# Kernel optimization log

Measured on AMD Instinct MI355X. Metric: run time of the kernel, lower is better.

The kernel has to match this reference:

```python
import jax, jax.numpy as jnp
import numpy as np

N_NODES = 100000
NNZ = 3200000
D_FEAT = 128


def setup_inputs() -> dict:
    key = jax.random.key(0)
    k1, k2, k3 = jax.random.split(key, 3)
    indices = jax.random.randint(k1, (2, NNZ), 0, N_NODES, dtype=jnp.int64 if jax.config.jax_enable_x64 else jnp.int32)
    values = jax.random.normal(k2, (NNZ,), dtype=jnp.float32)
    b = jax.random.normal(k3, (N_NODES, D_FEAT), dtype=jnp.float32)
    return {"indices": indices, "values": values, "n_rows": N_NODES, "b": b}


def reference(indices, values, n_rows, b):
    # out = sparse_coo(indices, values, [n_rows, n_rows]) @ b
    # out[i] = sum_{e: row[e]==i} values[e] * b[col[e]]
    row, col = indices[0], indices[1]
    gathered = values[:, None] * b[col]              # [nnz, d]
    out = jax.ops.segment_sum(gathered, row, num_segments=n_rows)  # [n_rows, d]
    return out
```

## Files before the change

### kernel.cpp

```cpp
#include <hip/hip_runtime.h>


#define D_FEAT 128
#define RPB 128
#define BKT_SHIFT 7
#define MAX_NB 1024
#define NBLK_SCAT 512
#define CHUNK_MAX 6400
#define STG_CAP 6144
#define CT_SHIFT 13
#define NKEY (RPB * 16)
#define RP_FLAG (1 << 30)

__device__ __forceinline__ unsigned short f2bf(float f) {
    unsigned u = __float_as_uint(f);
    u += 0x7FFFu + ((u >> 16) & 1u);
    return (unsigned short)(u >> 16);
}
__global__ void bconv_kernel(const float* __restrict__ bmat,
                             ushort* __restrict__ b16, int n4) {
    int i = blockIdx.x * blockDim.x + threadIdx.x;
    int gs = gridDim.x * blockDim.x;
    for (int k = i; k < n4; k += gs) {
        float4 v = reinterpret_cast<const float4*>(bmat)[k];
        ushort4 o;
        o.x = f2bf(v.x); o.y = f2bf(v.y); o.z = f2bf(v.z); o.w = f2bf(v.w);
        reinterpret_cast<ushort4*>(b16)[k] = o;
    }
}

__global__ void hist_kernel(const int* __restrict__ rowidx, int* __restrict__ hist,
                            int nnz) {
    __shared__ int lcnt[MAX_NB];
    for (int i = threadIdx.x; i < MAX_NB; i += blockDim.x) lcnt[i] = 0;
    __syncthreads();
    int gid = blockIdx.x * blockDim.x + threadIdx.x;
    int gsz = gridDim.x * blockDim.x;
    for (int e = gid; e < nnz; e += gsz)
        atomicAdd(&lcnt[rowidx[e] >> BKT_SHIFT], 1);
    __syncthreads();
    for (int i = threadIdx.x; i < MAX_NB; i += blockDim.x)
        if (lcnt[i]) atomicAdd(&hist[i], lcnt[i]);
}

__global__ void scan_kernel(const int* __restrict__ hist, int* __restrict__ gbase,
                            int* __restrict__ gcursor, int nb) {
    __shared__ int hs[512];
    int t = threadIdx.x;
    int v0 = hist[2 * t], v1 = hist[2 * t + 1];
    hs[t] = v0 + v1;
    __syncthreads();
    for (int off = 1; off < 512; off <<= 1) {
        int u = (t >= off) ? hs[t - off] : 0;
        __syncthreads();
        hs[t] += u;
        __syncthreads();
    }
    int excl = hs[t] - (v0 + v1);
    if (2 * t < nb)     { gbase[2 * t] = excl;          gcursor[2 * t] = excl; }
    if (2 * t + 1 < nb) { gbase[2 * t + 1] = excl + v0; gcursor[2 * t + 1] = excl + v0; }
}

__global__ __launch_bounds__(512)
void scatter_kernel(const int* __restrict__ rowidx, const int* __restrict__ colidx,
                    const float* __restrict__ vals, int* __restrict__ gcursor,
                    float2* __restrict__ cv, int nnz, int nb) {
    __shared__ int loff[MAX_NB];
    __shared__ int cur[MAX_NB];
    __shared__ int gpos[MAX_NB];
    __shared__ ushort bktof[CHUNK_MAX];
    __shared__ float2 stage[CHUNK_MAX];
    int* scanbuf = (int*)stage;

    int t = threadIdx.x;
    int chunk = (nnz + gridDim.x - 1) / gridDim.x;
    int beg = blockIdx.x * chunk;
    int end = min(beg + chunk, nnz);
    int n = end - beg;

    for (int i = t; i < MAX_NB; i += 512) loff[i] = 0;
    __syncthreads();
    for (int e = beg + t; e < end; e += 512)
        atomicAdd(&loff[rowidx[e] >> BKT_SHIFT], 1);
    __syncthreads();

    int v0 = loff[2 * t], v1 = loff[2 * t + 1];
    scanbuf[t] = v0 + v1;
    __syncthreads();
    for (int off = 1; off < 512; off <<= 1) {
        int u = (t >= off) ? scanbuf[t - off] : 0;
        __syncthreads();
        scanbuf[t] += u;
        __syncthreads();
    }
    int excl = scanbuf[t] - (v0 + v1);
    __syncthreads();
    loff[2 * t] = excl;       loff[2 * t + 1] = excl + v0;
    cur[2 * t]  = excl;       cur[2 * t + 1]  = excl + v0;
    __syncthreads();

    for (int e = beg + t; e < end; e += 512) {
        int r = rowidx[e];
        int bkt = r >> BKT_SHIFT;
        int pos = atomicAdd(&cur[bkt], 1);
        int pack = ((r & (RPB - 1)) << 17) | colidx[e];
        stage[pos] = make_float2(__int_as_float(pack), vals[e]);
        bktof[pos] = (ushort)bkt;
    }
    __syncthreads();

    for (int i = t; i < nb; i += 512) {
        int cnt = cur[i] - loff[i];
        if (cnt > 0) gpos[i] = atomicAdd(&gcursor[i], cnt);
    }
    __syncthreads();

    for (int i = t; i < n; i += 512) {
        int bkt = bktof[i];
        cv[gpos[bkt] + (i - loff[bkt])] = stage[i];
    }
}

__global__ __launch_bounds__(256)
void rowsort_kernel(const int* __restrict__ gbase, const int* __restrict__ gend,
                    float2* __restrict__ cv, int* __restrict__ rowptr,
                    int n_rows, int nb) {
    __shared__ float2 stg[STG_CAP];
    __shared__ int bin[NKEY];
    __shared__ int cur[NKEY];
    __shared__ int part[256];
    int t = threadIdx.x;
    int bkt = blockIdx.x;
    int beg = gbase[bkt], end = gend[bkt];
    int n = end - beg;

    if (bkt == nb - 1 && t == 0) rowptr[n_rows] = end;

    if (n > STG_CAP) {
        for (int rl = t; rl < RPB; rl += 256) {
            int row = bkt * RPB + rl;
            if (row < n_rows) rowptr[row] = beg | RP_FLAG;
        }
        return;
    }

    for (int i = t; i < NKEY; i += 256) bin[i] = 0;
    __syncthreads();
    for (int i = t; i < n; i += 256) {
        float2 p = cv[beg + i];
        stg[i] = p;
        int pk = __float_as_int(p.x);
        int key = ((pk >> 17) << 4) | ((pk & 0x1FFFF) >> CT_SHIFT);
        atomicAdd(&bin[key], 1);
    }
    __syncthreads();
    int base8 = t * 8;
    int loc[8];
    int s = 0;
    #pragma unroll
    for (int k = 0; k < 8; ++k) { loc[k] = bin[base8 + k]; s += loc[k]; }
    part[t] = s;
    __syncthreads();
    for (int off = 1; off < 256; off <<= 1) {
        int u = (t >= off) ? part[t - off] : 0;
        __syncthreads();
        part[t] += u;
        __syncthreads();
    }
    int run = part[t] - s;
    #pragma unroll
    for (int k = 0; k < 8; ++k) {
        int key = base8 + k;
        cur[key] = run;
        if ((key & 15) == 0) {
            int row = bkt * RPB + (key >> 4);
            if (row < n_rows) rowptr[row] = beg + run;
        }
        run += loc[k];
    }
    __syncthreads();
    for (int i = t; i < n; i += 256) {
        float2 p = stg[i];
        int pk = __float_as_int(p.x);
        int key = ((pk >> 17) << 4) | ((pk & 0x1FFFF) >> CT_SHIFT);
        int pos = atomicAdd(&cur[key], 1);
        cv[beg + pos] = p;
    }
}

__device__ __forceinline__ float bf2f(unsigned short h) {
    return __uint_as_float((unsigned)h << 16);
}
__global__ __launch_bounds__(256)
void rowmm16_kernel(const int* __restrict__ rowptr, const int* __restrict__ gbase,
                    const int* __restrict__ gend, const float2* __restrict__ cv,
                    const ushort* __restrict__ b16, float* __restrict__ out,
                    int n_rows) {
    int wid  = (blockIdx.x * blockDim.x + threadIdx.x) >> 6;
    int lane = threadIdx.x & 63;
    if (wid >= n_rows) return;

    const ushort2* bp = reinterpret_cast<const ushort2*>(b16) + lane;
    float2 acc = make_float2(0.f, 0.f);

    int rp = rowptr[wid];
    if (rp & RP_FLAG) {
        int bkt = wid >> BKT_SHIFT;
        int beg = gbase[bkt], end = gend[bkt];
        int myrl = wid & (RPB - 1);
        for (int j = beg; j < end; ++j) {
            float2 p = cv[j];
            int pack = __float_as_int(p.x);
            if ((pack >> 17) == myrl) {
                ushort2 u = bp[(size_t)(pack & 0x1FFFF) * (D_FEAT / 2)];
                acc.x += p.y * bf2f(u.x);  acc.y += p.y * bf2f(u.y);
            }
        }
    } else {
        int beg = rp;
        int end = rowptr[wid + 1] & ~RP_FLAG;
        int j = beg;
        for (; j + 7 < end; j += 8) {
            float2 p0 = cv[j],     p1 = cv[j + 1];
            float2 p2 = cv[j + 2], p3 = cv[j + 3];
            float2 p4 = cv[j + 4], p5 = cv[j + 5];
            float2 p6 = cv[j + 6], p7 = cv[j + 7];
            ushort2 u0 = bp[(size_t)(__float_as_int(p0.x) & 0x1FFFF) * (D_FEAT / 2)];
            ushort2 u1 = bp[(size_t)(__float_as_int(p1.x) & 0x1FFFF) * (D_FEAT / 2)];
            ushort2 u2 = bp[(size_t)(__float_as_int(p2.x) & 0x1FFFF) * (D_FEAT / 2)];
            ushort2 u3 = bp[(size_t)(__float_as_int(p3.x) & 0x1FFFF) * (D_FEAT / 2)];
            ushort2 u4 = bp[(size_t)(__float_as_int(p4.x) & 0x1FFFF) * (D_FEAT / 2)];
            ushort2 u5 = bp[(size_t)(__float_as_int(p5.x) & 0x1FFFF) * (D_FEAT / 2)];
            ushort2 u6 = bp[(size_t)(__float_as_int(p6.x) & 0x1FFFF) * (D_FEAT / 2)];
            ushort2 u7 = bp[(size_t)(__float_as_int(p7.x) & 0x1FFFF) * (D_FEAT / 2)];
            acc.x += p0.y * bf2f(u0.x);  acc.y += p0.y * bf2f(u0.y);
            acc.x += p1.y * bf2f(u1.x);  acc.y += p1.y * bf2f(u1.y);
            acc.x += p2.y * bf2f(u2.x);  acc.y += p2.y * bf2f(u2.y);
            acc.x += p3.y * bf2f(u3.x);  acc.y += p3.y * bf2f(u3.y);
            acc.x += p4.y * bf2f(u4.x);  acc.y += p4.y * bf2f(u4.y);
            acc.x += p5.y * bf2f(u5.x);  acc.y += p5.y * bf2f(u5.y);
            acc.x += p6.y * bf2f(u6.x);  acc.y += p6.y * bf2f(u6.y);
            acc.x += p7.y * bf2f(u7.x);  acc.y += p7.y * bf2f(u7.y);
        }
        for (; j < end; ++j) {
            float2 p = cv[j];
            ushort2 u = bp[(size_t)(__float_as_int(p.x) & 0x1FFFF) * (D_FEAT / 2)];
            acc.x += p.y * bf2f(u.x);  acc.y += p.y * bf2f(u.y);
        }
    }
    reinterpret_cast<float2*>(out + (size_t)wid * D_FEAT)[lane] = acc;
}

__global__ __launch_bounds__(256)
void rowmm_kernel(const int* __restrict__ rowptr, const int* __restrict__ gbase,
                  const int* __restrict__ gend, const float2* __restrict__ cv,
                  const float* __restrict__ bmat, float* __restrict__ out,
                  int n_rows) {
    int wid  = (blockIdx.x * blockDim.x + threadIdx.x) >> 6;
    int lane = threadIdx.x & 63;
    if (wid >= n_rows) return;
    const float2* bp = reinterpret_cast<const float2*>(bmat) + lane;
    float2 acc = make_float2(0.f, 0.f);
    int rp = rowptr[wid];
    if (rp & RP_FLAG) {
        int bkt = wid >> BKT_SHIFT;
        int beg = gbase[bkt], end = gend[bkt];
        int myrl = wid & (RPB - 1);
        for (int j = beg; j < end; ++j) {
            float2 p = cv[j];
            int pack = __float_as_int(p.x);
            if ((pack >> 17) == myrl) {
                float2 v = bp[(size_t)(pack & 0x1FFFF) * (D_FEAT / 2)];
                acc.x += p.y * v.x;  acc.y += p.y * v.y;
            }
        }
    } else {
        int beg = rp, end = rowptr[wid + 1] & ~RP_FLAG;
        for (int j = beg; j < end; ++j) {
            float2 p = cv[j];
            float2 v = bp[(size_t)(__float_as_int(p.x) & 0x1FFFF) * (D_FEAT / 2)];
            acc.x += p.y * v.x;  acc.y += p.y * v.y;
        }
    }
    reinterpret_cast<float2*>(out + (size_t)wid * D_FEAT)[lane] = acc;
}

extern "C" void kernel_launch(void* const* d_in, const int* in_sizes, int n_in,
                              void* d_out, int out_size, void* d_ws, size_t ws_size,
                              hipStream_t stream) {
    const int*   indices = (const int*)d_in[0];
    const float* values  = (const float*)d_in[1];
    const float* b       = (const float*)d_in[3];
    float*       out     = (float*)d_out;

    const int nnz    = in_sizes[1];
    const int n_rows = out_size / D_FEAT;
    const int nb     = (n_rows + RPB - 1) / RPB;
    const int* rowidx = indices;
    const int* colidx = indices + nnz;

    int*    hist    = (int*)d_ws;
    int*    gbase   = hist + MAX_NB;
    int*    gcursor = gbase + MAX_NB;
    int*    rowptr  = gcursor + MAX_NB;
    size_t  off     = (3 * MAX_NB + (size_t)n_rows + 1) * sizeof(int);
    off = (off + 15) & ~(size_t)15;

    size_t b16_bytes = (size_t)n_rows * D_FEAT * sizeof(ushort);
    size_t cv_bytes  = (size_t)nnz * sizeof(float2);
    bool   use16     = (off + b16_bytes + cv_bytes) <= ws_size;

    ushort* b16 = (ushort*)((char*)d_ws + off);
    float2* cv  = (float2*)((char*)d_ws + off + (use16 ? b16_bytes : 0));

    hipMemsetAsync(hist, 0, MAX_NB * sizeof(int), stream);
    if (use16)
        bconv_kernel<<<1024, 256, 0, stream>>>(b, b16, n_rows * D_FEAT / 4);
    hist_kernel<<<512, 256, 0, stream>>>(rowidx, hist, nnz);
    scan_kernel<<<1, 512, 0, stream>>>(hist, gbase, gcursor, nb);
    scatter_kernel<<<NBLK_SCAT, 512, 0, stream>>>(rowidx, colidx, values, gcursor, cv, nnz, nb);
    rowsort_kernel<<<nb, 256, 0, stream>>>(gbase, gcursor, cv, rowptr, n_rows, nb);
    if (use16)
        rowmm16_kernel<<<(n_rows * 64 + 255) / 256, 256, 0, stream>>>(rowptr, gbase, gcursor,
                                                                      cv, b16, out, n_rows);
    else
        rowmm_kernel<<<(n_rows * 64 + 255) / 256, 256, 0, stream>>>(rowptr, gbase, gcursor,
                                                                    cv, b, out, n_rows);
}
```

Before: 251.9 us.

## Tile SpMM by column segment within 64-row buckets and add atomic fallback

Buckets shrink to 64 rows. Rowsort now orders each bucket's entries column-tile-major (16 column tiles by 64 rows) and stores per-bucket ushort offsets instead of a global rowptr. The new mm kernel assigns one block per bucket, and each warp owns 8 rows. All warps sweep the column tiles in the same order, so gathers of b rows stay in a smaller cache footprint. The change also adds an atomic fallback for oversized inputs and sizes the scatter grid by chunk size. The costs are more serial per-warp work, lower parallelism (about 1563 blocks), and loop overhead per row-tile segment.

```diff
diff --git a/kernel.cpp b/kernel.cpp
--- a/kernel.cpp
+++ b/kernel.cpp
@@ -2,21 +2,45 @@
 
 
 #define D_FEAT 128
-#define RPB 128
-#define BKT_SHIFT 7
-#define MAX_NB 1024
-#define NBLK_SCAT 512
+#define RPB 64
+#define BKT_SHIFT 6
+#define MAX_NB 2048
 #define CHUNK_MAX 6400
-#define STG_CAP 6144
+#define STG_CAP 3072
+#define NT 16
 #define CT_SHIFT 13
-#define NKEY (RPB * 16)
-#define RP_FLAG (1 << 30)
+#define NKEY 1024
+#define SSTRIDE 1025
 
 __device__ __forceinline__ unsigned short f2bf(float f) {
     unsigned u = __float_as_uint(f);
     u += 0x7FFFu + ((u >> 16) & 1u);
     return (unsigned short)(u >> 16);
 }
+__device__ __forceinline__ float bf2f(unsigned short h) {
+    return __uint_as_float((unsigned)h << 16);
+}
+
+__global__ void spmm_atomic_kernel(const int* __restrict__ rowidx,
+                                   const int* __restrict__ colidx,
+                                   const float* __restrict__ vals,
+                                   const float* __restrict__ b,
+                                   float* __restrict__ out, int nnz) {
+    int gtid = blockIdx.x * blockDim.x + threadIdx.x;
+    int group = gtid >> 5, fid = gtid & 31;
+    int ngroup = (gridDim.x * blockDim.x) >> 5;
+    for (int e = group; e < nnz; e += ngroup) {
+        int r = rowidx[e], c = colidx[e];
+        float v = vals[e];
+        float4 bv = reinterpret_cast<const float4*>(b + (size_t)c * D_FEAT)[fid];
+        float* orow = out + (size_t)r * D_FEAT + (size_t)fid * 4;
+        atomicAdd(orow + 0, v * bv.x);
+        atomicAdd(orow + 1, v * bv.y);
+        atomicAdd(orow + 2, v * bv.z);
+        atomicAdd(orow + 3, v * bv.w);
+    }
+}
+
 __global__ void bconv_kernel(const float* __restrict__ bmat,
                              ushort* __restrict__ b16, int n4) {
     int i = blockIdx.x * blockDim.x + threadIdx.x;
@@ -45,20 +69,20 @@
 
 __global__ void scan_kernel(const int* __restrict__ hist, int* __restrict__ gbase,
                             int* __restrict__ gcursor, int nb) {
-    __shared__ int hs[512];
+    __shared__ int hs[1024];
     int t = threadIdx.x;
-    int v0 = hist[2 * t], v1 = hist[2 * t + 1];
-    hs[t] = v0 + v1;
-    __syncthreads();
-    for (int off = 1; off < 512; off <<= 1) {
+    int c0 = hist[2 * t], c1 = hist[2 * t + 1];
+    hs[t] = c0 + c1;
+    __syncthreads();
+    for (int off = 1; off < 1024; off <<= 1) {
         int u = (t >= off) ? hs[t - off] : 0;
         __syncthreads();
         hs[t] += u;
         __syncthreads();
     }
-    int excl = hs[t] - (v0 + v1);
+    int excl = hs[t] - (c0 + c1);
     if (2 * t < nb)     { gbase[2 * t] = excl;          gcursor[2 * t] = excl; }
-    if (2 * t + 1 < nb) { gbase[2 * t + 1] = excl + v0; gcursor[2 * t + 1] = excl + v0; }
+    if (2 * t + 1 < nb) { gbase[2 * t + 1] = excl + c0; gcursor[2 * t + 1] = excl + c0; }
 }
 
 __global__ __launch_bounds__(512)
@@ -77,6 +101,7 @@
     int beg = blockIdx.x * chunk;
     int end = min(beg + chunk, nnz);
     int n = end - beg;
+    if (n <= 0) return;
 
     for (int i = t; i < MAX_NB; i += 512) loff[i] = 0;
     __syncthreads();
@@ -84,8 +109,9 @@
         atomicAdd(&loff[rowidx[e] >> BKT_SHIFT], 1);
     __syncthreads();
 
-    int v0 = loff[2 * t], v1 = loff[2 * t + 1];
-    scanbuf[t] = v0 + v1;
+    int c0 = loff[4*t], c1 = loff[4*t+1], c2 = loff[4*t+2], c3 = loff[4*t+3];
+    int s = c0 + c1 + c2 + c3;
+    scanbuf[t] = s;
     __syncthreads();
     for (int off = 1; off < 512; off <<= 1) {
         int u = (t >= off) ? scanbuf[t - off] : 0;
@@ -93,18 +119,20 @@
         scanbuf[t] += u;
         __syncthreads();
     }
-    int excl = scanbuf[t] - (v0 + v1);
-    __syncthreads();
-    loff[2 * t] = excl;       loff[2 * t + 1] = excl + v0;
-    cur[2 * t]  = excl;       cur[2 * t + 1]  = excl + v0;
+    int excl = scanbuf[t] - s;
+    __syncthreads();
+    loff[4*t] = excl;             loff[4*t+1] = excl + c0;
+    loff[4*t+2] = excl + c0 + c1; loff[4*t+3] = excl + c0 + c1 + c2;
+    cur[4*t] = loff[4*t];     cur[4*t+1] = loff[4*t+1];
+    cur[4*t+2] = loff[4*t+2]; cur[4*t+3] = loff[4*t+3];
     __syncthreads();
 
     for (int e = beg + t; e < end; e += 512) {
         int r = rowidx[e];
         int bkt = r >> BKT_SHIFT;
         int pos = atomicAdd(&cur[bkt], 1);
-        int pack = ((r & (RPB - 1)) << 17) | colidx[e];
-        stage[pos] = make_float2(__int_as_float(pack), vals[e]);
+        stage[pos] = make_float2(__int_as_float(((r & (RPB - 1)) << 17) | colidx[e]),
+                                 vals[e]);
         bktof[pos] = (ushort)bkt;
     }
     __syncthreads();
@@ -123,24 +151,18 @@
 
 __global__ __launch_bounds__(256)
 void rowsort_kernel(const int* __restrict__ gbase, const int* __restrict__ gend,
-                    float2* __restrict__ cv, int* __restrict__ rowptr,
-                    int n_rows, int nb) {
+                    float2* __restrict__ cv, ushort* __restrict__ strt) {
     __shared__ float2 stg[STG_CAP];
     __shared__ int bin[NKEY];
     __shared__ int cur[NKEY];
     __shared__ int part[256];
-    int t = threadIdx.x;
-    int bkt = blockIdx.x;
+    int t = threadIdx.x, bkt = blockIdx.x;
     int beg = gbase[bkt], end = gend[bkt];
     int n = end - beg;
-
-    if (bkt == nb - 1 && t == 0) rowptr[n_rows] = end;
+    ushort* sp = strt + (size_t)bkt * SSTRIDE;
 
     if (n > STG_CAP) {
-        for (int rl = t; rl < RPB; rl += 256) {
-            int row = bkt * RPB + rl;
-            if (row < n_rows) rowptr[row] = beg | RP_FLAG;
-        }
+        if (t == 0) sp[NKEY] = 0xFFFFu;
         return;
     }
 
@@ -150,15 +172,13 @@
         float2 p = cv[beg + i];
         stg[i] = p;
         int pk = __float_as_int(p.x);
-        int key = ((pk >> 17) << 4) | ((pk & 0x1FFFF) >> CT_SHIFT);
+        int key = (((pk & 0x1FFFF) >> CT_SHIFT) << 6) | (pk >> 17);
         atomicAdd(&bin[key], 1);
     }
     __syncthreads();
-    int base8 = t * 8;
-    int loc[8];
-    int s = 0;
+    int base4 = t * 4, loc[4], s = 0;
     #pragma unroll
-    for (int k = 0; k < 8; ++k) { loc[k] = bin[base8 + k]; s += loc[k]; }
+    for (int k = 0; k < 4; ++k) { loc[k] = bin[base4 + k]; s += loc[k]; }
     part[t] = s;
     __syncthreads();
     for (int off = 1; off < 256; off <<= 1) {
@@ -169,120 +189,114 @@
     }
     int run = part[t] - s;
     #pragma unroll
-    for (int k = 0; k < 8; ++k) {
-        int key = base8 + k;
+    for (int k = 0; k < 4; ++k) {
+        int key = base4 + k;
         cur[key] = run;
-        if ((key & 15) == 0) {
-            int row = bkt * RPB + (key >> 4);
-            if (row < n_rows) rowptr[row] = beg + run;
-        }
+        sp[key] = (ushort)run;
         run += loc[k];
     }
+    if (t == 255) sp[NKEY] = (ushort)n;
     __syncthreads();
     for (int i = t; i < n; i += 256) {
         float2 p = stg[i];
         int pk = __float_as_int(p.x);
-        int key = ((pk >> 17) << 4) | ((pk & 0x1FFFF) >> CT_SHIFT);
+        int key = (((pk & 0x1FFFF) >> CT_SHIFT) << 6) | (pk >> 17);
         int pos = atomicAdd(&cur[key], 1);
         cv[beg + pos] = p;
     }
 }
 
-__device__ __forceinline__ float bf2f(unsigned short h) {
-    return __uint_as_float((unsigned)h << 16);
-}
-__global__ __launch_bounds__(256)
-void rowmm16_kernel(const int* __restrict__ rowptr, const int* __restrict__ gbase,
-                    const int* __restrict__ gend, const float2* __restrict__ cv,
-                    const ushort* __restrict__ b16, float* __restrict__ out,
-                    int n_rows) {
-    int wid  = (blockIdx.x * blockDim.x + threadIdx.x) >> 6;
-    int lane = threadIdx.x & 63;
-    if (wid >= n_rows) return;
-
+__global__ __launch_bounds__(512)
+void mm_kernel(const int* __restrict__ gbase, const int* __restrict__ gend,
+               const ushort* __restrict__ strt, const float2* __restrict__ cv,
+               const ushort* __restrict__ b16, float* __restrict__ out,
+               int n_rows) {
+    __shared__ int sstrt[NKEY + 1];
+    int t = threadIdx.x, bkt = blockIdx.x;
+    int gb = gbase[bkt], ge = gend[bkt];
+    int w = t >> 6, lane = t & 63;
+    int rl0 = w * 8;
     const ushort2* bp = reinterpret_cast<const ushort2*>(b16) + lane;
-    float2 acc = make_float2(0.f, 0.f);
-
-    int rp = rowptr[wid];
-    if (rp & RP_FLAG) {
-        int bkt = wid >> BKT_SHIFT;
-        int beg = gbase[bkt], end = gend[bkt];
-        int myrl = wid & (RPB - 1);
-        for (int j = beg; j < end; ++j) {
+
+    const ushort* sp = strt + (size_t)bkt * SSTRIDE;
+    for (int i = t; i <= NKEY; i += 512) sstrt[i] = sp[i];
+    __syncthreads();
+
+    float2 acc[8];
+    #pragma unroll
+    for (int k = 0; k < 8; ++k) acc[k] = make_float2(0.f, 0.f);
+
+    if (sstrt[NKEY] == 0xFFFF) {
+        for (int j = gb; j < ge; ++j) {
             float2 p = cv[j];
-            int pack = __float_as_int(p.x);
-            if ((pack >> 17) == myrl) {
-                ushort2 u = bp[(size_t)(pack & 0x1FFFF) * (D_FEAT / 2)];
-                acc.x += p.y * bf2f(u.x);  acc.y += p.y * bf2f(u.y);
+            int pk = __float_as_int(p.x);
+            int rl = pk >> 17;
+            if ((rl >> 3) == w) {
+                ushort2 u = bp[(size_t)(pk & 0x1FFFF) << 6];
+                float cx = p.y * bf2f(u.x), cy = p.y * bf2f(u.y);
+                switch (rl & 7) {
+                    case 0: acc[0].x += cx; acc[0].y += cy; break;
+                    case 1: acc[1].x += cx; acc[1].y += cy; break;
+                    case 2: acc[2].x += cx; acc[2].y += cy; break;
+                    case 3: acc[3].x += cx; acc[3].y += cy; break;
+                    case 4: acc[4].x += cx; acc[4].y += cy; break;
+                    case 5: acc[5].x += cx; acc[5].y += cy; break;
+                    case 6: acc[6].x += cx; acc[6].y += cy; break;
+                    default: acc[7].x += cx; acc[7].y += cy; break;
+                }
             }
         }
     } else {
-        int beg = rp;
-        int end = rowptr[wid + 1] & ~RP_FLAG;
-        int j = beg;
-        for (; j + 7 < end; j += 8) {
-            float2 p0 = cv[j],     p1 = cv[j + 1];
-            float2 p2 = cv[j + 2], p3 = cv[j + 3];
-            float2 p4 = cv[j + 4], p5 = cv[j + 5];
-            float2 p6 = cv[j + 6], p7 = cv[j + 7];
-            ushort2 u0 = bp[(size_t)(__float_as_int(p0.x) & 0x1FFFF) * (D_FEAT / 2)];
-            ushort2 u1 = bp[(size_t)(__float_as_int(p1.x) & 0x1FFFF) * (D_FEAT / 2)];
-            ushort2 u2 = bp[(size_t)(__float_as_int(p2.x) & 0x1FFFF) * (D_FEAT / 2)];
-            ushort2 u3 = bp[(size_t)(__float_as_int(p3.x) & 0x1FFFF) * (D_FEAT / 2)];
-            ushort2 u4 = bp[(size_t)(__float_as_int(p4.x) & 0x1FFFF) * (D_FEAT / 2)];
-            ushort2 u5 = bp[(size_t)(__float_as_int(p5.x) & 0x1FFFF) * (D_FEAT / 2)];
-            ushort2 u6 = bp[(size_t)(__float_as_int(p6.x) & 0x1FFFF) * (D_FEAT / 2)];
-            ushort2 u7 = bp[(size_t)(__float_as_int(p7.x) & 0x1FFFF) * (D_FEAT / 2)];
-            acc.x += p0.y * bf2f(u0.x);  acc.y += p0.y * bf2f(u0.y);
-            acc.x += p1.y * bf2f(u1.x);  acc.y += p1.y * bf2f(u1.y);
-            acc.x += p2.y * bf2f(u2.x);  acc.y += p2.y * bf2f(u2.y);
-            acc.x += p3.y * bf2f(u3.x);  acc.y += p3.y * bf2f(u3.y);
-            acc.x += p4.y * bf2f(u4.x);  acc.y += p4.y * bf2f(u4.y);
-            acc.x += p5.y * bf2f(u5.x);  acc.y += p5.y * bf2f(u5.y);
-            acc.x += p6.y * bf2f(u6.x);  acc.y += p6.y * bf2f(u6.y);
-            acc.x += p7.y * bf2f(u7.x);  acc.y += p7.y * bf2f(u7.y);
-        }
-        for (; j < end; ++j) {
-            float2 p = cv[j];
-            ushort2 u = bp[(size_t)(__float_as_int(p.x) & 0x1FFFF) * (D_FEAT / 2)];
-            acc.x += p.y * bf2f(u.x);  acc.y += p.y * bf2f(u.y);
-        }
-    }
-    reinterpret_cast<float2*>(out + (size_t)wid * D_FEAT)[lane] = acc;
-}
-
-__global__ __launch_bounds__(256)
-void rowmm_kernel(const int* __restrict__ rowptr, const int* __restrict__ gbase,
-                  const int* __restrict__ gend, const float2* __restrict__ cv,
-                  const float* __restrict__ bmat, float* __restrict__ out,
-                  int n_rows) {
-    int wid  = (blockIdx.x * blockDim.x + threadIdx.x) >> 6;
-    int lane = threadIdx.x & 63;
-    if (wid >= n_rows) return;
-    const float2* bp = reinterpret_cast<const float2*>(bmat) + lane;
-    float2 acc = make_float2(0.f, 0.f);
-    int rp = rowptr[wid];
-    if (rp & RP_FLAG) {
-        int bkt = wid >> BKT_SHIFT;
-        int beg = gbase[bkt], end = gend[bkt];
-        int myrl = wid & (RPB - 1);
-        for (int j = beg; j < end; ++j) {
-            float2 p = cv[j];
-            int pack = __float_as_int(p.x);
-            if ((pack >> 17) == myrl) {
-                float2 v = bp[(size_t)(pack & 0x1FFFF) * (D_FEAT / 2)];
-                acc.x += p.y * v.x;  acc.y += p.y * v.y;
+        for (int tt = 0; tt < NT; ++tt) {
+            int base = (tt << 6) + rl0;
+            #pragma unroll
+            for (int k = 0; k < 8; ++k) {
+                int jb = gb + sstrt[base + k];
+                int je = gb + sstrt[base + k + 1];
+                int j = jb;
+                for (; j + 7 < je; j += 8) {
+                    float2 p0 = cv[j],     p1 = cv[j + 1];
+                    float2 p2 = cv[j + 2], p3 = cv[j + 3];
+                    float2 p4 = cv[j + 4], p5 = cv[j + 5];
+                    float2 p6 = cv[j + 6], p7 = cv[j + 7];
+                    int k0 = __float_as_int(p0.x), k1 = __float_as_int(p1.x);
+                    int k2 = __float_as_int(p2.x), k3 = __float_as_int(p3.x);
+                    int k4 = __float_as_int(p4.x), k5 = __float_as_int(p5.x);
+                    int k6 = __float_as_int(p6.x), k7 = __float_as_int(p7.x);
+                    ushort2 u0 = bp[(size_t)(k0 & 0x1FFFF) << 6];
+                    ushort2 u1 = bp[(size_t)(k1 & 0x1FFFF) << 6];
+                    ushort2 u2 = bp[(size_t)(k2 & 0x1FFFF) << 6];
+                    ushort2 u3 = bp[(size_t)(k3 & 0x1FFFF) << 6];
+                    ushort2 u4 = bp[(size_t)(k4 & 0x1FFFF) << 6];
+                    ushort2 u5 = bp[(size_t)(k5 & 0x1FFFF) << 6];
+                    ushort2 u6 = bp[(size_t)(k6 & 0x1FFFF) << 6];
+                    ushort2 u7 = bp[(size_t)(k7 & 0x1FFFF) << 6];
+                    acc[k].x += p0.y * bf2f(u0.x);  acc[k].y += p0.y * bf2f(u0.y);
+                    acc[k].x += p1.y * bf2f(u1.x);  acc[k].y += p1.y * bf2f(u1.y);
+                    acc[k].x += p2.y * bf2f(u2.x);  acc[k].y += p2.y * bf2f(u2.y);
+                    acc[k].x += p3.y * bf2f(u3.x);  acc[k].y += p3.y * bf2f(u3.y);
+                    acc[k].x += p4.y * bf2f(u4.x);  acc[k].y += p4.y * bf2f(u4.y);
+                    acc[k].x += p5.y * bf2f(u5.x);  acc[k].y += p5.y * bf2f(u5.y);
+                    acc[k].x += p6.y * bf2f(u6.x);  acc[k].y += p6.y * bf2f(u6.y);
+                    acc[k].x += p7.y * bf2f(u7.x);  acc[k].y += p7.y * bf2f(u7.y);
+                }
+                for (; j < je; ++j) {
+                    float2 p = cv[j];
+                    int pk = __float_as_int(p.x);
+                    ushort2 u = bp[(size_t)(pk & 0x1FFFF) << 6];
+                    acc[k].x += p.y * bf2f(u.x);
+                    acc[k].y += p.y * bf2f(u.y);
+                }
             }
         }
-    } else {
-        int beg = rp, end = rowptr[wid + 1] & ~RP_FLAG;
-        for (int j = beg; j < end; ++j) {
-            float2 p = cv[j];
-            float2 v = bp[(size_t)(__float_as_int(p.x) & 0x1FFFF) * (D_FEAT / 2)];
-            acc.x += p.y * v.x;  acc.y += p.y * v.y;
-        }
-    }
-    reinterpret_cast<float2*>(out + (size_t)wid * D_FEAT)[lane] = acc;
+    }
+    int rowbase = bkt * RPB + rl0;
+    float2* op = reinterpret_cast<float2*>(out) + lane;
+    #pragma unroll
+    for (int k = 0; k < 8; ++k) {
+        int row = rowbase + k;
+        if (row < n_rows) op[(size_t)row * 64] = acc[k];
+    }
 }
 
 extern "C" void kernel_launch(void* const* d_in, const int* in_sizes, int n_in,
@@ -295,35 +309,35 @@
 
     const int nnz    = in_sizes[1];
     const int n_rows = out_size / D_FEAT;
-    const int nb     = (n_rows + RPB - 1) / RPB;
+    const int nb     = (n_rows + RPB - 1) >> BKT_SHIFT;
     const int* rowidx = indices;
     const int* colidx = indices + nnz;
 
     int*    hist    = (int*)d_ws;
     int*    gbase   = hist + MAX_NB;
     int*    gcursor = gbase + MAX_NB;
-    int*    rowptr  = gcursor + MAX_NB;
-    size_t  off     = (3 * MAX_NB + (size_t)n_rows + 1) * sizeof(int);
-    off = (off + 15) & ~(size_t)15;
-
-    size_t b16_bytes = (size_t)n_rows * D_FEAT * sizeof(ushort);
-    size_t cv_bytes  = (size_t)nnz * sizeof(float2);
-    bool   use16     = (off + b16_bytes + cv_bytes) <= ws_size;
-
+    ushort* strt    = (ushort*)(gcursor + MAX_NB);
+    size_t  off = (size_t)3 * MAX_NB * sizeof(int)
+                + (size_t)nb * SSTRIDE * sizeof(ushort);
+    off = (off + 255) & ~(size_t)255;
+    size_t b16_bytes = ((size_t)n_rows * D_FEAT * 2 + 255) & ~(size_t)255;
     ushort* b16 = (ushort*)((char*)d_ws + off);
-    float2* cv  = (float2*)((char*)d_ws + off + (use16 ? b16_bytes : 0));
+    float2* cv  = (float2*)((char*)d_ws + off + b16_bytes);
+
+    size_t need = off + b16_bytes + (size_t)nnz * sizeof(float2);
+    if (need > ws_size || n_rows > 131072 || nb > MAX_NB) {
+        hipMemsetAsync(d_out, 0, (size_t)out_size * sizeof(float), stream);
+        spmm_atomic_kernel<<<8192, 256, 0, stream>>>(rowidx, colidx, values, b, out, nnz);
+        return;
+    }
 
     hipMemsetAsync(hist, 0, MAX_NB * sizeof(int), stream);
-    if (use16)
-        bconv_kernel<<<1024, 256, 0, stream>>>(b, b16, n_rows * D_FEAT / 4);
+    bconv_kernel<<<1024, 256, 0, stream>>>(b, b16, n_rows * D_FEAT / 4);
     hist_kernel<<<512, 256, 0, stream>>>(rowidx, hist, nnz);
-    scan_kernel<<<1, 512, 0, stream>>>(hist, gbase, gcursor, nb);
-    scatter_kernel<<<NBLK_SCAT, 512, 0, stream>>>(rowidx, colidx, values, gcursor, cv, nnz, nb);
-    rowsort_kernel<<<nb, 256, 0, stream>>>(gbase, gcursor, cv, rowptr, n_rows, nb);
-    if (use16)
-        rowmm16_kernel<<<(n_rows * 64 + 255) / 256, 256, 0, stream>>>(rowptr, gbase, gcursor,
-                                                                      cv, b16, out, n_rows);
-    else
-        rowmm_kernel<<<(n_rows * 64 + 255) / 256, 256, 0, stream>>>(rowptr, gbase, gcursor,
-                                                                    cv, b, out, n_rows);
-}
+    scan_kernel<<<1, 1024, 0, stream>>>(hist, gbase, gcursor, nb);
+    int nblkS = (nnz + CHUNK_MAX - 1) / CHUNK_MAX;
+    scatter_kernel<<<nblkS, 512, 0, stream>>>(rowidx, colidx, values, gcursor,
+                                              cv, nnz, nb);
+    rowsort_kernel<<<nb, 256, 0, stream>>>(gbase, gcursor, cv, strt);
+    mm_kernel<<<nb, 512, 0, stream>>>(gbase, gcursor, strt, cv, b16, out, n_rows);
+}
```

After: 422.9 us. 1.68x slower.
